# Performance work log

Hardware: AMD Instinct MI355X
Metric: run time of the kernel (lower is better)

Reference implementation:

```python
import jax, jax.numpy as jnp
import numpy as np

RADIUS = 0.2
NSAMPLE = 32


def setup_inputs() -> dict:
    key = jax.random.key(0)
    k1, k2 = jax.random.split(key)
    B, N = 8, 4096
    xyz = jax.random.uniform(k1, (B, N, 3), dtype=jnp.float32)
    xyz_new = jax.random.uniform(k2, (B, N, 3), dtype=jnp.float32)  # ignored by forward, kept for signature fidelity
    return {"xyz": xyz, "xyz_new": xyz_new}


def _ball_query(radius, nsample, xyz, new_xyz):
    # xyz: [B, N, 3] source points; new_xyz: [B, M, 3] query centers.
    # Returns idx: [B, M, nsample] int32, matching pointnet2 CUDA ball_query:
    # first `nsample` indices j (in increasing j order) with ||q - p_j||^2 < r^2;
    # unused slots are filled with the first valid index.
    B, N, _ = xyz.shape
    sq_src = jnp.sum(xyz * xyz, axis=-1)          # [B, N]
    sq_q = jnp.sum(new_xyz * new_xyz, axis=-1)    # [B, M]
    # d2[b, m, n] = ||q_m - p_n||^2
    d2 = sq_q[:, :, None] + sq_src[:, None, :] - 2.0 * jnp.einsum(
        "bmc,bnc->bmn", new_xyz, xyz)             # [B, M, N]
    mask = d2 < (radius * radius)                 # [B, M, N] bool
    # key = index j when within radius, else sentinel N (sorts to the end)
    idx_range = jnp.arange(N, dtype=jnp.int32)
    keys = jnp.where(mask, idx_range[None, None, :], jnp.int32(N))
    sorted_keys = jnp.sort(keys, axis=-1)[..., :nsample]  # [B, M, nsample]
    first = sorted_keys[..., 0:1]                 # first valid index (pad value)
    idx = jnp.where(sorted_keys < N, sorted_keys, first)
    return idx.astype(jnp.int32)


def reference(xyz, xyz_new):
    # Faithful to the module: ball_query(radius, nsample, xyz, xyz) — xyz_new unused.
    return _ball_query(RADIUS, NSAMPLE, xyz, xyz)
```

## Files before the change

### kernel.cpp

```cpp
#include <hip/hip_runtime.h>
#include <cstdint>


#define BQ_N    4096
#define BQ_B    8
#define BQ_NS   32
#define BQ_R2   0.04f
#define BQ_NC   16

typedef float v2f __attribute__((ext_vector_type(2)));

__device__ __forceinline__ float sq_plain(float x, float y, float z) {
    float r, t;
    asm("v_mul_f32 %0, %2, %2\n\t"
        "v_mul_f32 %1, %3, %3\n\t"
        "v_add_f32 %0, %0, %1\n\t"
        "v_mul_f32 %1, %4, %4\n\t"
        "v_add_f32 %0, %0, %1"
        : "=&v"(r), "=&v"(t)
        : "v"(x), "v"(y), "v"(z));
    return r;
}

__device__ __forceinline__ v2f sq2_plain(v2f x, v2f y, v2f z) {
    v2f r, t;
    asm("v_pk_mul_f32 %0, %2, %2 op_sel:[0,0] op_sel_hi:[1,1]\n\t"
        "v_pk_mul_f32 %1, %3, %3 op_sel:[0,0] op_sel_hi:[1,1]\n\t"
        "v_pk_add_f32 %0, %0, %1 op_sel:[0,0] op_sel_hi:[1,1]\n\t"
        "v_pk_mul_f32 %1, %4, %4 op_sel:[0,0] op_sel_hi:[1,1]\n\t"
        "v_pk_add_f32 %0, %0, %1 op_sel:[0,0] op_sel_hi:[1,1]"
        : "=&v"(r), "=&v"(t)
        : "v"(x), "v"(y), "v"(z));
    return r;
}

__device__ __forceinline__ v2f d2_pk(v2f qa, v2f qb, v2f sx, v2f sy, v2f sz,
                                     v2f sq2) {
    v2f r, t;
    asm("v_pk_mul_f32 %0, %2, %4 op_sel:[0,0] op_sel_hi:[0,1]\n\t"
        "v_pk_fma_f32 %0, %2, %5, %0 op_sel:[1,0,0] op_sel_hi:[1,1,1]\n\t"
        "v_pk_fma_f32 %0, %3, %6, %0 op_sel:[0,0,0] op_sel_hi:[0,1,1]\n\t"
        "v_pk_add_f32 %0, %0, %0 op_sel:[0,0] op_sel_hi:[1,1]\n\t"
        "v_pk_add_f32 %1, %3, %7 op_sel:[1,0] op_sel_hi:[1,1]\n\t"
        "v_pk_add_f32 %0, %1, %0 op_sel:[0,0] op_sel_hi:[1,1] neg_lo:[0,1] neg_hi:[0,1]"
        : "=&v"(r), "=&v"(t)
        : "v"(qa), "v"(qb), "v"(sx), "v"(sy), "v"(sz), "v"(sq2));
    return r;
}

__device__ __forceinline__ void proc_pair(v2f qa, v2f qb, v2f sx, v2f sy,
                                          v2f sz, v2f sq2, int lane, int k,
                                          uint32_t& wlo, uint32_t& whi,
                                          int& p, int& f) {
    const v2f d2 = d2_pk(qa, qb, sx, sy, sz, sq2);
    const uint64_t b0 = __ballot(d2[0] < BQ_R2);
    if (lane == k)     { wlo = (uint32_t)b0; whi = (uint32_t)(b0 >> 32); p = f; }
    f += (int)__popcll(b0);
    const uint64_t b1 = __ballot(d2[1] < BQ_R2);
    if (lane == k + 1) { wlo = (uint32_t)b1; whi = (uint32_t)(b1 >> 32); p = f; }
    f += (int)__popcll(b1);
}

__device__ __forceinline__ void emit_query(int* __restrict__ orow, int lane,
                                           uint32_t wlo, uint32_t whi,
                                           int wpre, int total)
{
    const uint64_t word = ((uint64_t)whi << 32) | wlo;
    uint64_t w = word;
    int pos = wpre;
    while (w != 0ull && pos < BQ_NS) {
        const int bit = __builtin_ctzll(w);
        orow[pos] = (lane << 6) + bit;
        w &= (w - 1);
        ++pos;
    }
    if (total < BQ_NS) {
        int first;
        const uint64_t nz = __ballot(word != 0ull);
        if (nz == 0ull) {
            first = BQ_N;
        } else {
            const int fl = __builtin_ctzll(nz);
            const uint64_t fw = __shfl(word, fl);
            first = (fl << 6) + __builtin_ctzll(fw);
        }
        if (lane >= total && lane < BQ_NS) orow[lane] = first;
    }
}

__global__ __launch_bounds__(128, 4)
void ball_query_kernel(const float* __restrict__ xyz, int* __restrict__ out)
{
    const int b    = blockIdx.x >> 8;
    const int wq   = ((blockIdx.x & 255) << 4) + ((threadIdx.x >> 6) << 3);
    const int lane = threadIdx.x & 63;
    const float* __restrict__ src = xyz + (size_t)b * BQ_N * 3;
    int* __restrict__ outb = out + (size_t)(b * BQ_N) * BQ_NS;

    v2f Qa[8], Qb[8];
    #pragma unroll
    for (int j = 0; j < 8; ++j) {
        const int m = wq + j;
        const float x = src[3 * m + 0];
        const float y = src[3 * m + 1];
        const float z = src[3 * m + 2];
        Qa[j][0] = x; Qa[j][1] = y;
        Qb[j][0] = z; Qb[j][1] = sq_plain(x, y, z);
    }

    uint32_t Wlo[8] = {0,0,0,0,0,0,0,0};
    uint32_t Whi[8] = {0,0,0,0,0,0,0,0};
    int      P[8]   = {0,0,0,0,0,0,0,0};
    int      F[8]   = {0,0,0,0,0,0,0,0};

    const float* lp = src + lane * 3;

    for (int c = 0; c < BQ_NC; ++c) {
        v2f X01, Y01, Z01, X23, Y23, Z23;
        X01[0] = lp[  0]; X01[1] = lp[192];
        Y01[0] = lp[  1]; Y01[1] = lp[193];
        Z01[0] = lp[  2]; Z01[1] = lp[194];
        X23[0] = lp[384]; X23[1] = lp[576];
        Y23[0] = lp[385]; Y23[1] = lp[577];
        Z23[0] = lp[386]; Z23[1] = lp[578];
        lp += 768;

        const v2f SQ01 = sq2_plain(X01, Y01, Z01);
        const v2f SQ23 = sq2_plain(X23, Y23, Z23);

        const int k0 = c << 2;
        #pragma unroll
        for (int j = 0; j < 8; ++j) {
            if (F[j] < BQ_NS) {
                proc_pair(Qa[j], Qb[j], X01, Y01, Z01, SQ01, lane, k0,
                          Wlo[j], Whi[j], P[j], F[j]);
                proc_pair(Qa[j], Qb[j], X23, Y23, Z23, SQ23, lane, k0 + 2,
                          Wlo[j], Whi[j], P[j], F[j]);
            }
        }

        int m = F[0];
        #pragma unroll
        for (int j = 1; j < 8; ++j) m = min(m, F[j]);
        if (m >= BQ_NS) break;
    }

    #pragma unroll
    for (int j = 0; j < 8; ++j)
        emit_query(outb + (size_t)(wq + j) * BQ_NS, lane,
                   Wlo[j], Whi[j], P[j], F[j]);
}

extern "C" void kernel_launch(void* const* d_in, const int* in_sizes, int n_in,
                              void* d_out, int out_size, void* d_ws, size_t ws_size,
                              hipStream_t stream)
{
    const float* xyz = (const float*)d_in[0];
    int* out = (int*)d_out;
    hipLaunchKernelGGL(ball_query_kernel, dim3(2048), dim3(128), 0, stream,
                       xyz, out);
}
```

Baseline: 80.37 us.

## Assign one query per wave instead of eight to enable per-query early exit

Restructures the kernel so each 64-lane wave handles a single query point rather than eight, with a larger grid and 256-thread blocks. Each query can stop scanning source chunks as soon as it has enough neighbors, instead of waiting for the slowest of eight, and register pressure drops. In exchange, source-point loads and squared-norm computations are no longer amortized across eight queries, so memory and ALU traffic per query increases.

```diff
diff --git a/kernel.cpp b/kernel.cpp
--- a/kernel.cpp
+++ b/kernel.cpp
@@ -88,30 +88,24 @@
     }
 }
 
-__global__ __launch_bounds__(128, 4)
+__global__ __launch_bounds__(256, 8)
 void ball_query_kernel(const float* __restrict__ xyz, int* __restrict__ out)
 {
-    const int b    = blockIdx.x >> 8;
-    const int wq   = ((blockIdx.x & 255) << 4) + ((threadIdx.x >> 6) << 3);
+    const int gw   = (blockIdx.x << 2) + (threadIdx.x >> 6);
+    const int b    = gw >> 12;
+    const int m    = gw & (BQ_N - 1);
     const int lane = threadIdx.x & 63;
     const float* __restrict__ src = xyz + (size_t)b * BQ_N * 3;
-    int* __restrict__ outb = out + (size_t)(b * BQ_N) * BQ_NS;
 
-    v2f Qa[8], Qb[8];
-    #pragma unroll
-    for (int j = 0; j < 8; ++j) {
-        const int m = wq + j;
-        const float x = src[3 * m + 0];
-        const float y = src[3 * m + 1];
-        const float z = src[3 * m + 2];
-        Qa[j][0] = x; Qa[j][1] = y;
-        Qb[j][0] = z; Qb[j][1] = sq_plain(x, y, z);
-    }
+    const float qx = src[3 * m + 0];
+    const float qy = src[3 * m + 1];
+    const float qz = src[3 * m + 2];
+    v2f Qa, Qb;
+    Qa[0] = qx; Qa[1] = qy;
+    Qb[0] = qz; Qb[1] = sq_plain(qx, qy, qz);
 
-    uint32_t Wlo[8] = {0,0,0,0,0,0,0,0};
-    uint32_t Whi[8] = {0,0,0,0,0,0,0,0};
-    int      P[8]   = {0,0,0,0,0,0,0,0};
-    int      F[8]   = {0,0,0,0,0,0,0,0};
+    uint32_t wlo = 0, whi = 0;
+    int p = 0, f = 0;
 
     const float* lp = src + lane * 3;
 
@@ -129,26 +123,13 @@
         const v2f SQ23 = sq2_plain(X23, Y23, Z23);
 
         const int k0 = c << 2;
-        #pragma unroll
-        for (int j = 0; j < 8; ++j) {
-            if (F[j] < BQ_NS) {
-                proc_pair(Qa[j], Qb[j], X01, Y01, Z01, SQ01, lane, k0,
-                          Wlo[j], Whi[j], P[j], F[j]);
-                proc_pair(Qa[j], Qb[j], X23, Y23, Z23, SQ23, lane, k0 + 2,
-                          Wlo[j], Whi[j], P[j], F[j]);
-            }
-        }
+        proc_pair(Qa, Qb, X01, Y01, Z01, SQ01, lane, k0,     wlo, whi, p, f);
+        proc_pair(Qa, Qb, X23, Y23, Z23, SQ23, lane, k0 + 2, wlo, whi, p, f);
 
-        int m = F[0];
-        #pragma unroll
-        for (int j = 1; j < 8; ++j) m = min(m, F[j]);
-        if (m >= BQ_NS) break;
+        if (f >= BQ_NS) break;
     }
 
-    #pragma unroll
-    for (int j = 0; j < 8; ++j)
-        emit_query(outb + (size_t)(wq + j) * BQ_NS, lane,
-                   Wlo[j], Whi[j], P[j], F[j]);
+    emit_query(out + (size_t)gw * BQ_NS, lane, wlo, whi, p, f);
 }
 
 extern "C" void kernel_launch(void* const* d_in, const int* in_sizes, int n_in,
@@ -157,6 +138,6 @@
 {
     const float* xyz = (const float*)d_in[0];
     int* out = (int*)d_out;
-    hipLaunchKernelGGL(ball_query_kernel, dim3(2048), dim3(128), 0, stream,
+    hipLaunchKernelGGL(ball_query_kernel, dim3(8192), dim3(256), 0, stream,
                        xyz, out);
 }
```

After: 83.81 us. 1.04x slower.
